# Performance work log

Measured on AMD Instinct MI355X. Metric: run time of the kernel, lower is better.

The kernel has to match this reference:

```python
import jax, jax.numpy as jnp
import numpy as np

D_K = 64


def setup_inputs() -> dict:
    key = jax.random.key(0)
    kq, kk, kv = jax.random.split(key, 3)
    B, H, S, D = 4, 16, 2048, 64
    return {
        "query": jax.random.normal(kq, (B, H, S, D), dtype=jnp.float32),
        "key": jax.random.normal(kk, (B, H, S, D), dtype=jnp.float32),
        "value": jax.random.normal(kv, (B, H, S, D), dtype=jnp.float32),
        "to_mask": 1,
    }


def reference(query, key, value, to_mask):
    # QK^T / sqrt(d_k): [B,H,S,S]
    scores = jnp.einsum("bhqd,bhkd->bhqk", query, key) / jnp.sqrt(
        jnp.asarray(D_K, dtype=query.dtype)
    )
    if to_mask:
        S = scores.shape[-1]
        # upper-triangular (strictly above diagonal) gets large negative bias
        causal = jnp.triu(jnp.ones((S, S), dtype=scores.dtype), k=1)
        scores = scores + causal[None, None, :, :] * jnp.asarray(-1e19, scores.dtype)
    attn = jax.nn.softmax(scores, axis=-1)
    return jnp.einsum("bhqk,bhkd->bhqd", attn, value)
```

## Files before the change

kernel.cpp:

```cpp
#include <hip/hip_runtime.h>
#include <math.h>

#define S_LEN 2048
#define D_HEAD 64
#define NT 32
#define BM 256
#define BN 64
#define NQT (S_LEN / BM)
#define TILE_HALFS 4096
#define PSTRIDE 72
#define QSCALE (0.125f * 1.44269504088896340736f)

typedef _Float16 f16;
typedef f16 f16x4 __attribute__((ext_vector_type(4)));
typedef f16 f16x8 __attribute__((ext_vector_type(8)));
typedef float f32x4 __attribute__((ext_vector_type(4)));

#define ASYNC16(g, l)                                                          \
    __builtin_amdgcn_global_load_lds(                                          \
        (const __attribute__((address_space(1))) void*)(g),                    \
        (__attribute__((address_space(3))) void*)(l), 16, 0, 0)

__global__ __launch_bounds__(256)
void prepass_kernel(const float* __restrict__ K, const float* __restrict__ V,
                    f16* __restrict__ Kw, f16* __restrict__ Vw) {
    const int kt = blockIdx.x, bh = blockIdx.y, tid = threadIdx.x;
    const int t = tid >> 6, lane = tid & 63, c = lane & 15, quad = lane >> 4;
    const size_t gbase = (size_t)bh * S_LEN * D_HEAD + (size_t)kt * BN * D_HEAD;
    const size_t tb = ((size_t)bh * NT + kt) * TILE_HALFS;

    __shared__ float Vt_s[64][65];

    float4 vv[4];
    #pragma unroll
    for (int i = 0; i < 4; ++i) {
        const int fi = tid + i * 256;
        const int row = fi >> 4, d0 = (fi & 15) * 4;
        vv[i] = *(const float4*)(V + gbase + row * 64 + d0);
    }

    #pragma unroll
    for (int ch = 0; ch < 2; ++ch) {
        const float* src = K + gbase + (size_t)(t * 16 + c) * 64 + ch * 32 + quad * 8;
        const float4 a = *(const float4*)src;
        const float4 b = *(const float4*)(src + 4);
        f16 h[8];
        h[0] = (f16)a.x; h[1] = (f16)a.y; h[2] = (f16)a.z; h[3] = (f16)a.w;
        h[4] = (f16)b.x; h[5] = (f16)b.y; h[6] = (f16)b.z; h[7] = (f16)b.w;
        *(f16x8*)&Kw[tb + (size_t)((t * 2 + ch) * 64 + lane) * 8] = *(f16x8*)h;
    }

    #pragma unroll
    for (int i = 0; i < 4; ++i) {
        const int fi = tid + i * 256;
        const int row = fi >> 4, d0 = (fi & 15) * 4;
        Vt_s[row][d0 + 0] = vv[i].x; Vt_s[row][d0 + 1] = vv[i].y;
        Vt_s[row][d0 + 2] = vv[i].z; Vt_s[row][d0 + 3] = vv[i].w;
    }
    __syncthreads();
    #pragma unroll
    for (int tp = 0; tp < 2; ++tp) {
        f16 h[8];
        #pragma unroll
        for (int u = 0; u < 2; ++u)
            #pragma unroll
            for (int j = 0; j < 4; ++j)
                h[4 * u + j] = (f16)Vt_s[tp * 32 + u * 16 + quad * 4 + j][t * 16 + c];
        *(f16x8*)&Vw[tb + (size_t)((t * 2 + tp) * 64 + lane) * 8] = *(f16x8*)h;
    }
}

__global__ __launch_bounds__(512, 4)
void fa_fwd_kernel(const float* __restrict__ Q, const f16* __restrict__ Kw,
                   const f16* __restrict__ Vw, const int* __restrict__ to_mask,
                   float* __restrict__ O) {
    const int linear = (int)blockIdx.x;
    const int g      = linear >> 3;
    const int idx    = g >> 3;
    const int qt     = (idx < 4) ? (7 - idx) : (idx - 4);
    const int bh     = (linear & 7) + 8 * (g & 7);

    const int tid  = threadIdx.x;
    const int wave = tid >> 6;
    const int lane = tid & 63;
    const int c    = lane & 15;
    const int quad = lane >> 4;
    const int i0   = qt * BM;
    const int wrow0 = i0 + wave * 32;

    const int mask_on = to_mask[0];
    const int kt_end  = mask_on ? (4 * qt + 3) : (NT - 1);

    __shared__ __align__(16) f16 KV[4][2][TILE_HALFS];

    const size_t base  = (size_t)bh * S_LEN * D_HEAD;
    const size_t tbase = (size_t)bh * NT * TILE_HALFS;

    f16x8 aq[2][2];
    #pragma unroll
    for (int set = 0; set < 2; ++set) {
        const float* qp = Q + base + (size_t)(wrow0 + set * 16 + c) * D_HEAD + quad * 8;
        #pragma unroll
        for (int ch = 0; ch < 2; ++ch) {
            const float4 a = *(const float4*)(qp + ch * 32);
            const float4 b = *(const float4*)(qp + ch * 32 + 4);
            aq[set][ch][0] = (f16)(a.x * QSCALE); aq[set][ch][1] = (f16)(a.y * QSCALE);
            aq[set][ch][2] = (f16)(a.z * QSCALE); aq[set][ch][3] = (f16)(a.w * QSCALE);
            aq[set][ch][4] = (f16)(b.x * QSCALE); aq[set][ch][5] = (f16)(b.y * QSCALE);
            aq[set][ch][6] = (f16)(b.z * QSCALE); aq[set][ch][7] = (f16)(b.w * QSCALE);
        }
    }

    f32x4 o[2][4];
    f32x4 accl[2];
    #pragma unroll
    for (int set = 0; set < 2; ++set) {
        accl[set] = (f32x4){0.f, 0.f, 0.f, 0.f};
        #pragma unroll
        for (int nt = 0; nt < 4; ++nt) o[set][nt] = (f32x4){0.f, 0.f, 0.f, 0.f};
    }

    const f16 one1 = (f16)1.0f;
    const f16x4 ones4 = {one1, one1, one1, one1};

    asm volatile("s_waitcnt vmcnt(0)" ::: "memory");

    ASYNC16(Kw + tbase + wave * 512 + lane * 8, &KV[0][0][wave * 512]);
    ASYNC16(Vw + tbase + wave * 512 + lane * 8, &KV[0][1][wave * 512]);
    ASYNC16(Kw + tbase + TILE_HALFS + wave * 512 + lane * 8, &KV[1][0][wave * 512]);
    ASYNC16(Vw + tbase + TILE_HALFS + wave * 512 + lane * 8, &KV[1][1][wave * 512]);
    ASYNC16(Kw + tbase + 2 * TILE_HALFS + wave * 512 + lane * 8, &KV[2][0][wave * 512]);
    ASYNC16(Vw + tbase + 2 * TILE_HALFS + wave * 512 + lane * 8, &KV[2][1][wave * 512]);

    for (int kt = 0; kt <= kt_end; ++kt) {
        asm volatile("s_waitcnt vmcnt(4)" ::: "memory");
        __builtin_amdgcn_s_barrier();
        __builtin_amdgcn_sched_barrier(0);

        {
            const int pf = (kt + 3 <= kt_end) ? (kt + 3) : kt_end;
            const size_t tb = tbase + (size_t)pf * TILE_HALFS;
            f16* lk = &KV[(kt + 3) & 3][0][0];
            f16* lv = &KV[(kt + 3) & 3][1][0];
            ASYNC16(Kw + tb + wave * 512 + lane * 8, lk + wave * 512);
            ASYNC16(Vw + tb + wave * 512 + lane * 8, lv + wave * 512);
        }

        const int j0 = kt * BN;
        if (mask_on && j0 > wrow0 + 31) continue;

        const f16* Kt = &KV[kt & 3][0][0];
        const f16* Vv = &KV[kt & 3][1][0];

        f32x4 s[2][4];
        #pragma unroll
        for (int t = 0; t < 4; ++t) {
            const f16x8 kf0 = *(const f16x8*)&Kt[(t * 2 + 0) * 512 + lane * 8];
            const f16x8 kf1 = *(const f16x8*)&Kt[(t * 2 + 1) * 512 + lane * 8];
            #pragma unroll
            for (int set = 0; set < 2; ++set) {
                f32x4 acc = (f32x4){0.f, 0.f, 0.f, 0.f};
                acc = __builtin_amdgcn_mfma_f32_16x16x32_f16(kf0, aq[set][0], acc, 0, 0, 0);
                acc = __builtin_amdgcn_mfma_f32_16x16x32_f16(kf1, aq[set][1], acc, 0, 0, 0);
                s[set][t] = acc;
            }
        }

        if (mask_on && j0 + 63 > wrow0) {
            #pragma unroll
            for (int set = 0; set < 2; ++set)
                #pragma unroll
                for (int t = 0; t < 4; ++t)
                    #pragma unroll
                    for (int r = 0; r < 4; ++r)
                        if (j0 + t * 16 + quad * 4 + r > wrow0 + set * 16 + c)
                            s[set][t][r] = -1e30f;
        }

        f16x4 pq[2][4];
        #pragma unroll
        for (int set = 0; set < 2; ++set)
            #pragma unroll
            for (int t2 = 0; t2 < 4; ++t2) {
                f16x4 p;
                #pragma unroll
                for (int r = 0; r < 4; ++r)
                    p[r] = (f16)__builtin_amdgcn_exp2f(fminf(s[set][t2][r], 15.0f));
                pq[set][t2] = p;
            }

        #pragma unroll
        for (int set = 0; set < 2; ++set)
            #pragma unroll
            for (int t2 = 0; t2 < 4; ++t2)
                accl[set] = __builtin_amdgcn_mfma_f32_16x16x16f16(pq[set][t2], ones4, accl[set], 0, 0, 0);

        #pragma unroll
        for (int nt = 0; nt < 4; ++nt) {
            #pragma unroll
            for (int tp = 0; tp < 2; ++tp) {
                const f16x8 bvp = *(const f16x8*)&Vv[(nt * 2 + tp) * 512 + lane * 8];
                const f16x4 bv0 = {bvp[0], bvp[1], bvp[2], bvp[3]};
                const f16x4 bv1 = {bvp[4], bvp[5], bvp[6], bvp[7]};
                #pragma unroll
                for (int set = 0; set < 2; ++set) {
                    o[set][nt] = __builtin_amdgcn_mfma_f32_16x16x16f16(pq[set][2 * tp + 0], bv0, o[set][nt], 0, 0, 0);
                    o[set][nt] = __builtin_amdgcn_mfma_f32_16x16x16f16(pq[set][2 * tp + 1], bv1, o[set][nt], 0, 0, 0);
                }
            }
        }
    }

    asm volatile("s_waitcnt vmcnt(0)" ::: "memory");

    #pragma unroll
    for (int set = 0; set < 2; ++set)
        #pragma unroll
        for (int r = 0; r < 4; ++r) {
            const float inv = 1.0f / accl[set][r];
            float* op = O + base + (size_t)(wrow0 + set * 16 + quad * 4 + r) * D_HEAD;
            #pragma unroll
            for (int nt = 0; nt < 4; ++nt)
                op[nt * 16 + c] = o[set][nt][r] * inv;
        }
}

__global__ __launch_bounds__(256)
void fa_fwd_fallback(const float* __restrict__ Q, const float* __restrict__ K,
                     const float* __restrict__ V, const int* __restrict__ to_mask,
                     float* __restrict__ O) {
    const int qt = blockIdx.x, bh = blockIdx.y, tid = threadIdx.x;
    const int wave = tid >> 6, lane = tid & 63, c = lane & 15, quad = lane >> 4;
    const int i0 = qt * 64;
    const int mask_on = to_mask[0];
    const int kt_end = mask_on ? qt : (NT - 1);
    __shared__ __align__(16) f16 Ks[64][PSTRIDE];
    __shared__ __align__(16) f16 Vs[64][PSTRIDE];
    __shared__ __align__(16) f16 Psf[64][PSTRIDE];
    const size_t base = (size_t)bh * S_LEN * D_HEAD;
    f16x8 aq[2];
    {
        const float* qp = Q + base + (size_t)(i0 + wave * 16 + c) * D_HEAD + quad * 8;
        for (int ch = 0; ch < 2; ++ch)
            for (int j = 0; j < 8; ++j) aq[ch][j] = (f16)(qp[ch * 32 + j] * 0.125f);
    }
    f32x4 o[4]; float m_run[4], l_run[4], alpha_r[4];
    for (int t = 0; t < 4; ++t) o[t] = (f32x4){0.f, 0.f, 0.f, 0.f};
    for (int r = 0; r < 4; ++r) { m_run[r] = -INFINITY; l_run[r] = 0.f; }
    for (int kt = 0; kt <= kt_end; ++kt) {
        const int j0 = kt * 64;
        __syncthreads();
        for (int i = 0; i < 4; ++i) {
            const int f = tid + i * 256, key = f >> 4, d = (f & 15) * 4;
            const float4 kv = *(const float4*)(K + base + (size_t)(j0 + key) * D_HEAD + d);
            Ks[key][d] = (f16)kv.x; Ks[key][d + 1] = (f16)kv.y;
            Ks[key][d + 2] = (f16)kv.z; Ks[key][d + 3] = (f16)kv.w;
            const float4 vv = *(const float4*)(V + base + (size_t)(j0 + key) * D_HEAD + d);
            Vs[d][key] = (f16)vv.x; Vs[d + 1][key] = (f16)vv.y;
            Vs[d + 2][key] = (f16)vv.z; Vs[d + 3][key] = (f16)vv.w;
        }
        __syncthreads();
        f32x4 s[4];
        for (int t = 0; t < 4; ++t) {
            f32x4 acc = (f32x4){0.f, 0.f, 0.f, 0.f};
            const f16x8 b0 = *(const f16x8*)&Ks[t * 16 + c][quad * 8];
            const f16x8 b1 = *(const f16x8*)&Ks[t * 16 + c][32 + quad * 8];
            acc = __builtin_amdgcn_mfma_f32_16x16x32_f16(aq[0], b0, acc, 0, 0, 0);
            acc = __builtin_amdgcn_mfma_f32_16x16x32_f16(aq[1], b1, acc, 0, 0, 0);
            s[t] = acc;
        }
        if (mask_on && kt == qt)
            for (int t = 0; t < 4; ++t)
                for (int r = 0; r < 4; ++r)
                    if (t * 16 + c > wave * 16 + quad * 4 + r) s[t][r] = -1e30f;
        for (int r = 0; r < 4; ++r) {
            float mx = fmaxf(fmaxf(s[0][r], s[1][r]), fmaxf(s[2][r], s[3][r]));
            mx = fmaxf(mx, __shfl_xor(mx, 1)); mx = fmaxf(mx, __shfl_xor(mx, 2));
            mx = fmaxf(mx, __shfl_xor(mx, 4)); mx = fmaxf(mx, __shfl_xor(mx, 8));
            const float m_new = fmaxf(m_run[r], mx);
            const float alpha = __expf(m_run[r] - m_new);
            m_run[r] = m_new;
            float rs = 0.f;
            for (int t = 0; t < 4; ++t) { const float p = __expf(s[t][r] - m_new); s[t][r] = p; rs += p; }
            rs += __shfl_xor(rs, 1); rs += __shfl_xor(rs, 2);
            rs += __shfl_xor(rs, 4); rs += __shfl_xor(rs, 8);
            l_run[r] = l_run[r] * alpha + rs; alpha_r[r] = alpha;
        }
        for (int t = 0; t < 4; ++t)
            for (int r = 0; r < 4; ++r)
                Psf[wave * 16 + quad * 4 + r][t * 16 + c] = (f16)s[t][r];
        __syncthreads();
        const f16x8 ap0 = *(const f16x8*)&Psf[wave * 16 + c][quad * 8];
        const f16x8 ap1 = *(const f16x8*)&Psf[wave * 16 + c][32 + quad * 8];
        for (int t = 0; t < 4; ++t) {
            f32x4 acc = o[t];
            for (int r = 0; r < 4; ++r) acc[r] *= alpha_r[r];
            const f16x8 bv0 = *(const f16x8*)&Vs[t * 16 + c][quad * 8];
            const f16x8 bv1 = *(const f16x8*)&Vs[t * 16 + c][32 + quad * 8];
            acc = __builtin_amdgcn_mfma_f32_16x16x32_f16(ap0, bv0, acc, 0, 0, 0);
            acc = __builtin_amdgcn_mfma_f32_16x16x32_f16(ap1, bv1, acc, 0, 0, 0);
            o[t] = acc;
        }
    }
    for (int r = 0; r < 4; ++r) {
        const float inv = 1.f / l_run[r];
        float* op = O + base + (size_t)(i0 + wave * 16 + quad * 4 + r) * D_HEAD;
        for (int t = 0; t < 4; ++t) op[t * 16 + c] = o[t][r] * inv;
    }
}

extern "C" void kernel_launch(void* const* d_in, const int* in_sizes, int n_in,
                              void* d_out, int out_size, void* d_ws, size_t ws_size,
                              hipStream_t stream) {
    const float* Q = (const float*)d_in[0];
    const float* K = (const float*)d_in[1];
    const float* V = (const float*)d_in[2];
    const int* to_mask = (const int*)d_in[3];
    float* O = (float*)d_out;

    const size_t half_elems = (size_t)64 * S_LEN * D_HEAD;
    if (ws_size >= 2 * half_elems * sizeof(f16)) {
        f16* Kw = (f16*)d_ws;
        f16* Vw = Kw + half_elems;
        prepass_kernel<<<dim3(NT, 64), dim3(256), 0, stream>>>(K, V, Kw, Vw);
        fa_fwd_kernel<<<dim3(NQT * 64), dim3(512), 0, stream>>>(Q, Kw, Vw, to_mask, O);
    } else {
        fa_fwd_fallback<<<dim3(NT, 64), dim3(256), 0, stream>>>(Q, K, V, to_mask, O);
    }
}
```

Baseline: 181.9 us.

## Software-pipeline attention loop by deferring PV MFMAs to the next iteration

Restructures the KV loop so each phase runs the P·V and row-sum MFMAs for the previous tile alongside QK^T and exp for the current tile. Two P register buffers alternate across a two-phase unrolled loop, with a final drain step after the loop. The async prefetch distance drops from three tiles ahead to two, and the wait count changes to match. The aim is to overlap the exp/VALU work with matrix-core work, at the cost of more live registers and a shallower global-load lookahead.

```diff
diff --git a/kernel.cpp b/kernel.cpp
--- a/kernel.cpp
+++ b/kernel.cpp
@@ -123,93 +123,106 @@
     const f16 one1 = (f16)1.0f;
     const f16x4 ones4 = {one1, one1, one1, one1};
 
+    f16x4 pqA[2][4], pqB[2][4];
+
+#define DEFERRED(PQP, VPTR)                                                    \
+    {                                                                          \
+        const f16* Vp = (VPTR);                                                \
+        _Pragma("unroll")                                                      \
+        for (int set = 0; set < 2; ++set)                                      \
+            _Pragma("unroll")                                                  \
+            for (int t2 = 0; t2 < 4; ++t2)                                     \
+                accl[set] = __builtin_amdgcn_mfma_f32_16x16x16f16(PQP[set][t2], ones4, accl[set], 0, 0, 0); \
+        _Pragma("unroll")                                                      \
+        for (int nt = 0; nt < 4; ++nt) {                                       \
+            _Pragma("unroll")                                                  \
+            for (int tp = 0; tp < 2; ++tp) {                                   \
+                const f16x8 bvp = *(const f16x8*)&Vp[(nt * 2 + tp) * 512 + lane * 8]; \
+                const f16x4 bv0 = {bvp[0], bvp[1], bvp[2], bvp[3]};            \
+                const f16x4 bv1 = {bvp[4], bvp[5], bvp[6], bvp[7]};            \
+                _Pragma("unroll")                                              \
+                for (int set = 0; set < 2; ++set) {                            \
+                    o[set][nt] = __builtin_amdgcn_mfma_f32_16x16x16f16(PQP[set][2 * tp + 0], bv0, o[set][nt], 0, 0, 0); \
+                    o[set][nt] = __builtin_amdgcn_mfma_f32_16x16x16f16(PQP[set][2 * tp + 1], bv1, o[set][nt], 0, 0, 0); \
+                }                                                              \
+            }                                                                  \
+        }                                                                      \
+    }
+
+#define QKEXP(PQC, KTC)                                                        \
+    {                                                                          \
+        const f16* Kt = &KV[(KTC) & 3][0][0];                                  \
+        f32x4 s[2][4];                                                         \
+        _Pragma("unroll")                                                      \
+        for (int t = 0; t < 4; ++t) {                                          \
+            const f16x8 kf0 = *(const f16x8*)&Kt[(t * 2 + 0) * 512 + lane * 8]; \
+            const f16x8 kf1 = *(const f16x8*)&Kt[(t * 2 + 1) * 512 + lane * 8]; \
+            _Pragma("unroll")                                                  \
+            for (int set = 0; set < 2; ++set) {                                \
+                f32x4 acc = (f32x4){0.f, 0.f, 0.f, 0.f};                       \
+                acc = __builtin_amdgcn_mfma_f32_16x16x32_f16(kf0, aq[set][0], acc, 0, 0, 0); \
+                acc = __builtin_amdgcn_mfma_f32_16x16x32_f16(kf1, aq[set][1], acc, 0, 0, 0); \
+                s[set][t] = acc;                                               \
+            }                                                                  \
+        }                                                                      \
+        const int j0m = (KTC) * BN;                                            \
+        if (mask_on && j0m + 63 > wrow0) {                                     \
+            _Pragma("unroll")                                                  \
+            for (int set = 0; set < 2; ++set)                                  \
+                _Pragma("unroll")                                              \
+                for (int t = 0; t < 4; ++t)                                    \
+                    _Pragma("unroll")                                          \
+                    for (int r = 0; r < 4; ++r)                                \
+                        if (j0m + t * 16 + quad * 4 + r > wrow0 + set * 16 + c) \
+                            s[set][t][r] = -1e30f;                             \
+        }                                                                      \
+        _Pragma("unroll")                                                      \
+        for (int set = 0; set < 2; ++set)                                      \
+            _Pragma("unroll")                                                  \
+            for (int t2 = 0; t2 < 4; ++t2) {                                   \
+                f16x4 p;                                                       \
+                _Pragma("unroll")                                              \
+                for (int r = 0; r < 4; ++r)                                    \
+                    p[r] = (f16)__builtin_amdgcn_exp2f(fminf(s[set][t2][r], 15.0f)); \
+                PQC[set][t2] = p;                                              \
+            }                                                                  \
+    }
+
+#define PHASE(PQC, PQP, KT)                                                    \
+    {                                                                          \
+        const int kt_ = (KT);                                                  \
+        asm volatile("s_waitcnt vmcnt(2)" ::: "memory");                       \
+        __builtin_amdgcn_s_barrier();                                          \
+        __builtin_amdgcn_sched_barrier(0);                                     \
+        {                                                                      \
+            const int pf = (kt_ + 2 <= kt_end) ? (kt_ + 2) : kt_end;           \
+            const size_t tb = tbase + (size_t)pf * TILE_HALFS;                 \
+            f16* lk = &KV[(kt_ + 2) & 3][0][0];                                \
+            f16* lv = &KV[(kt_ + 2) & 3][1][0];                                \
+            ASYNC16(Kw + tb + wave * 512 + lane * 8, lk + wave * 512);         \
+            ASYNC16(Vw + tb + wave * 512 + lane * 8, lv + wave * 512);         \
+        }                                                                      \
+        if (kt_ > 0 && !(mask_on && (kt_ - 1) * BN > wrow0 + 31))              \
+            DEFERRED(PQP, &KV[(kt_ + 3) & 3][1][0]);                           \
+        if (!(mask_on && kt_ * BN > wrow0 + 31))                               \
+            QKEXP(PQC, kt_);                                                   \
+    }
+
     asm volatile("s_waitcnt vmcnt(0)" ::: "memory");
 
     ASYNC16(Kw + tbase + wave * 512 + lane * 8, &KV[0][0][wave * 512]);
     ASYNC16(Vw + tbase + wave * 512 + lane * 8, &KV[0][1][wave * 512]);
     ASYNC16(Kw + tbase + TILE_HALFS + wave * 512 + lane * 8, &KV[1][0][wave * 512]);
     ASYNC16(Vw + tbase + TILE_HALFS + wave * 512 + lane * 8, &KV[1][1][wave * 512]);
-    ASYNC16(Kw + tbase + 2 * TILE_HALFS + wave * 512 + lane * 8, &KV[2][0][wave * 512]);
-    ASYNC16(Vw + tbase + 2 * TILE_HALFS + wave * 512 + lane * 8, &KV[2][1][wave * 512]);
-
-    for (int kt = 0; kt <= kt_end; ++kt) {
-        asm volatile("s_waitcnt vmcnt(4)" ::: "memory");
-        __builtin_amdgcn_s_barrier();
-        __builtin_amdgcn_sched_barrier(0);
-
-        {
-            const int pf = (kt + 3 <= kt_end) ? (kt + 3) : kt_end;
-            const size_t tb = tbase + (size_t)pf * TILE_HALFS;
-            f16* lk = &KV[(kt + 3) & 3][0][0];
-            f16* lv = &KV[(kt + 3) & 3][1][0];
-            ASYNC16(Kw + tb + wave * 512 + lane * 8, lk + wave * 512);
-            ASYNC16(Vw + tb + wave * 512 + lane * 8, lv + wave * 512);
-        }
-
-        const int j0 = kt * BN;
-        if (mask_on && j0 > wrow0 + 31) continue;
-
-        const f16* Kt = &KV[kt & 3][0][0];
-        const f16* Vv = &KV[kt & 3][1][0];
-
-        f32x4 s[2][4];
-        #pragma unroll
-        for (int t = 0; t < 4; ++t) {
-            const f16x8 kf0 = *(const f16x8*)&Kt[(t * 2 + 0) * 512 + lane * 8];
-            const f16x8 kf1 = *(const f16x8*)&Kt[(t * 2 + 1) * 512 + lane * 8];
-            #pragma unroll
-            for (int set = 0; set < 2; ++set) {
-                f32x4 acc = (f32x4){0.f, 0.f, 0.f, 0.f};
-                acc = __builtin_amdgcn_mfma_f32_16x16x32_f16(kf0, aq[set][0], acc, 0, 0, 0);
-                acc = __builtin_amdgcn_mfma_f32_16x16x32_f16(kf1, aq[set][1], acc, 0, 0, 0);
-                s[set][t] = acc;
-            }
-        }
-
-        if (mask_on && j0 + 63 > wrow0) {
-            #pragma unroll
-            for (int set = 0; set < 2; ++set)
-                #pragma unroll
-                for (int t = 0; t < 4; ++t)
-                    #pragma unroll
-                    for (int r = 0; r < 4; ++r)
-                        if (j0 + t * 16 + quad * 4 + r > wrow0 + set * 16 + c)
-                            s[set][t][r] = -1e30f;
-        }
-
-        f16x4 pq[2][4];
-        #pragma unroll
-        for (int set = 0; set < 2; ++set)
-            #pragma unroll
-            for (int t2 = 0; t2 < 4; ++t2) {
-                f16x4 p;
-                #pragma unroll
-                for (int r = 0; r < 4; ++r)
-                    p[r] = (f16)__builtin_amdgcn_exp2f(fminf(s[set][t2][r], 15.0f));
-                pq[set][t2] = p;
-            }
-
-        #pragma unroll
-        for (int set = 0; set < 2; ++set)
-            #pragma unroll
-            for (int t2 = 0; t2 < 4; ++t2)
-                accl[set] = __builtin_amdgcn_mfma_f32_16x16x16f16(pq[set][t2], ones4, accl[set], 0, 0, 0);
-
-        #pragma unroll
-        for (int nt = 0; nt < 4; ++nt) {
-            #pragma unroll
-            for (int tp = 0; tp < 2; ++tp) {
-                const f16x8 bvp = *(const f16x8*)&Vv[(nt * 2 + tp) * 512 + lane * 8];
-                const f16x4 bv0 = {bvp[0], bvp[1], bvp[2], bvp[3]};
-                const f16x4 bv1 = {bvp[4], bvp[5], bvp[6], bvp[7]};
-                #pragma unroll
-                for (int set = 0; set < 2; ++set) {
-                    o[set][nt] = __builtin_amdgcn_mfma_f32_16x16x16f16(pq[set][2 * tp + 0], bv0, o[set][nt], 0, 0, 0);
-                    o[set][nt] = __builtin_amdgcn_mfma_f32_16x16x16f16(pq[set][2 * tp + 1], bv1, o[set][nt], 0, 0, 0);
-                }
-            }
-        }
-    }
+
+    const int nhalf = (kt_end + 1) >> 1;
+    for (int m = 0; m < nhalf; ++m) {
+        PHASE(pqA, pqB, 2 * m);
+        PHASE(pqB, pqA, 2 * m + 1);
+    }
+
+    if (!(mask_on && kt_end * BN > wrow0 + 31))
+        DEFERRED(pqB, &KV[kt_end & 3][1][0]);
 
     asm volatile("s_waitcnt vmcnt(0)" ::: "memory");
 
@@ -223,6 +236,10 @@
             for (int nt = 0; nt < 4; ++nt)
                 op[nt * 16 + c] = o[set][nt][r] * inv;
         }
+
+#undef DEFERRED
+#undef QKEXP
+#undef PHASE
 }
 
 __global__ __launch_bounds__(256)
```

After: 203.6 us. 12.0% more time.
